# Kernel tuning notes

Hardware: AMD Instinct MI355X
Metric: run time of the kernel (lower is better)

The kernel has to match this reference:

```python
import jax, jax.numpy as jnp
import numpy as np

N = 131072      # total nodes per (sub)graph batch
G = 1024        # number of graphs (= len(data.y))
NPG = N // G    # nodes per graph
E = 4194304     # edges per subgraph (avg degree 32)
D = 128         # input feature dim
LAT = (32, 32, 32)
HID = 128


def setup_inputs() -> dict:
    key = jax.random.key(0)
    ks = jax.random.split(key, 16)
    f = jnp.float32
    inp = {}
    for j in range(3):
        inp[f"x{j}"] = jax.random.normal(ks[j], (N, D), f)
        inp[f"edge_index{j}"] = jax.random.randint(ks[3 + j], (2, E), 0, N)
        inp[f"batch{j}"] = jnp.repeat(jnp.arange(G), NPG)  # sorted graph ids
    inp["y"] = jax.random.randint(ks[6], (G,), 0, 2)
    dims = [D] + list(LAT)
    for i in range(3):
        inp[f"Wc{i}"] = jax.random.normal(ks[7 + i], (dims[i], dims[i + 1]), f) / jnp.sqrt(jnp.asarray(dims[i], f))
        inp[f"bc{i}"] = jnp.zeros((dims[i + 1],), f)
    lat3 = sum(LAT) * 3
    inp["W1"] = jax.random.normal(ks[10], (lat3, HID), f) / jnp.sqrt(jnp.asarray(lat3, f))
    inp["b1"] = jnp.zeros((HID,), f)
    inp["W2"] = jax.random.normal(ks[11], (HID, 2), f) / jnp.sqrt(jnp.asarray(HID, f))
    inp["b2"] = jnp.zeros((2,), f)
    return inp


def gcn_conv(x, edge_index, W, b):
    """torch_geometric GCNConv: add self-loops + symmetric normalization."""
    n = x.shape[0]
    h = x @ W                                   # [N, out]
    src, dst = edge_index[0], edge_index[1]
    ones = jnp.ones(src.shape[0], h.dtype)
    deg = jax.ops.segment_sum(ones, dst, num_segments=n) + 1.0  # +1 self-loop
    dis = jax.lax.rsqrt(deg)                    # deg^{-1/2}
    norm = dis[src] * dis[dst]                  # [E]
    agg = jax.ops.segment_sum(h[src] * norm[:, None], dst, num_segments=n)
    return agg + h * (dis * dis)[:, None] + b   # self-loop term = h/deg


def branch(x, edge_index, batch, convs):
    h = x
    outs = []
    for (W, b) in convs:
        h = jnp.tanh(gcn_conv(h, edge_index, W, b))
        outs.append(h)
    feat = jnp.concatenate(outs, axis=1)        # [N, 96]
    # first node index of each graph (batch is sorted)
    idx = jnp.searchsorted(batch, jnp.arange(batch.shape[0] // NPG * 0 + G))
    return feat[idx]                            # [G, 96]


def reference(x0, edge_index0, batch0, x1, edge_index1, batch1,
              x2, edge_index2, batch2, y,
              Wc0, bc0, Wc1, bc1, Wc2, bc2, W1, b1, W2, b2):
    convs = [(Wc0, bc0), (Wc1, bc1), (Wc2, bc2)]  # shared across subgraphs
    feats = [branch(x, ei, b, convs)
             for (x, ei, b) in ((x0, edge_index0, batch0),
                                (x1, edge_index1, batch1),
                                (x2, edge_index2, batch2))]
    cat = jnp.concatenate(feats, axis=1)        # [G, 288]
    hidden = cat @ W1 + b1                      # [G, HID]
    feature = hidden
    h = jax.nn.relu(hidden)
    logits = jax.nn.log_softmax(h @ W2 + b2, axis=1)  # [G, 2]
    loss = -jnp.mean(logits[jnp.arange(G), y])  # nll_loss
    pred = jnp.argmax(logits, axis=1)
    acc = jnp.mean((pred == y).astype(jnp.float32))
    return logits, loss, acc, feature
```

## Files before the change

### kernel.cpp

```cpp
#include <hip/hip_runtime.h>
#include <hip/hip_bf16.h>
#include <hip/hip_fp16.h>

#define NN  131072
#define GG  1024
#define NPG 128
#define EE  4194304
#define DD  128
#define CC  32
#define NB  512
#define BTILE 4096
#define CAP 9600

typedef __hip_bfloat16 bf16;

__global__ void k_probe(const unsigned short* __restrict__ x, int* __restrict__ flag) {
    unsigned short u = x[threadIdx.x];
    int e = (u >> 7) & 0xFF;
    int q = (e >= 0x70 && e <= 0x85) ? 1 : 0;
    unsigned long long m = __ballot(q);
    __shared__ int cnt[2];
    if ((threadIdx.x & 63) == 0) cnt[threadIdx.x >> 6] = __popcll(m);
    __syncthreads();
    if (threadIdx.x == 0) flag[0] = (cnt[0] + cnt[1] >= 96) ? 1 : 0;
}

struct PtrPack { const void* p[10]; };
__global__ void k_cvtall(PtrPack pk, float* __restrict__ wf, const int* __restrict__ flag) {
    int i = blockIdx.x * 256 + threadIdx.x;
    if (i >= 43490) return;
    const int off[11] = {0, 4096, 4128, 5152, 5184, 6208, 6240, 43104, 43232, 43488, 43490};
    int seg = 0;
    #pragma unroll
    for (int k = 1; k < 11; k++) if (i >= off[k]) seg = k;
    int local = i - off[seg];
    if (flag[0]) wf[i] = __bfloat162float(((const bf16*)pk.p[seg])[local]);
    else         wf[i] = ((const float*)pk.p[seg])[local];
}


__global__ void __launch_bounds__(256) k_hist(const int* __restrict__ ei, int* __restrict__ bhist) {
    __shared__ int h[NB];
    int tid = threadIdx.x;
    h[tid] = 0; h[tid + 256] = 0;
    __syncthreads();
    long t0 = (long)blockIdx.x * 8192;
    #pragma unroll 4
    for (int k = 0; k < 32; k++) {
        int e = t0 + k * 256 + tid;
        atomicAdd(&h[ei[EE + e] >> 8], 1);
    }
    __syncthreads();
    atomicAdd(&bhist[tid], h[tid]);
    atomicAdd(&bhist[tid + 256], h[tid + 256]);
}

__global__ void __launch_bounds__(512) k_bscan(const int* __restrict__ bhist,
                                               int* __restrict__ bbase, int* __restrict__ bcur) {
    __shared__ int s[NB];
    int tid = threadIdx.x;
    int v = bhist[tid];
    s[tid] = v;
    __syncthreads();
    for (int o = 1; o < NB; o <<= 1) {
        int t = (tid >= o) ? s[tid - o] : 0;
        __syncthreads();
        s[tid] += t;
        __syncthreads();
    }
    bbase[tid] = s[tid] - v;
    bcur[tid] = s[tid] - v;
    if (tid == NB - 1) bbase[NB] = s[NB - 1];
}

__global__ void __launch_bounds__(512) k_bin(const int* __restrict__ ei,
                                             int* __restrict__ bcur, int2* __restrict__ ebuf) {
    __shared__ int hist[NB], loff[NB], gbase[NB], cur[NB];
    __shared__ int2 staged[BTILE];
    int tid = threadIdx.x;
    long t0 = (long)blockIdx.x * BTILE;
    hist[tid] = 0;
    __syncthreads();
    int sreg[BTILE / 512], dreg[BTILE / 512];
    #pragma unroll
    for (int k = 0; k < BTILE / 512; k++) {
        int e = t0 + k * 512 + tid;
        sreg[k] = ei[e];
        dreg[k] = ei[EE + e];
        atomicAdd(&hist[dreg[k] >> 8], 1);
    }
    __syncthreads();
    int v = hist[tid];
    loff[tid] = v;
    __syncthreads();
    for (int o = 1; o < NB; o <<= 1) {
        int t = (tid >= o) ? loff[tid - o] : 0;
        __syncthreads();
        loff[tid] += t;
        __syncthreads();
    }
    gbase[tid] = atomicAdd(&bcur[tid], v);
    cur[tid] = 0;
    int excl = loff[tid] - v;
    __syncthreads();
    loff[tid] = excl;
    __syncthreads();
    #pragma unroll
    for (int k = 0; k < BTILE / 512; k++) {
        int b = dreg[k] >> 8;
        int r = atomicAdd(&cur[b], 1);
        staged[loff[b] + r] = make_int2(dreg[k], sreg[k]);
    }
    __syncthreads();
    #pragma unroll
    for (int k = 0; k < BTILE / 512; k++) {
        int t = k * 512 + tid;
        int2 p = staged[t];
        int b = p.x >> 8;
        ebuf[gbase[b] + (t - loff[b])] = p;
    }
}

__global__ void __launch_bounds__(256) k_csr(const int* __restrict__ bbase,
                                             const int2* __restrict__ ebuf,
                                             int* __restrict__ rowptr, int* __restrict__ col,
                                             float* __restrict__ dis, int* __restrict__ mark) {
    __shared__ int hist[256], off[256], cur[256];
    __shared__ int lout[CAP];
    int b = blockIdx.x, tid = threadIdx.x;
    int base = bbase[b];
    int n = bbase[b + 1] - base;
    hist[tid] = 0;
    __syncthreads();
    for (int t = tid; t < n; t += 256) {
        int2 p = ebuf[base + t];
        atomicAdd(&hist[p.x & 255], 1);
    }
    __syncthreads();
    int deg = hist[tid];
    off[tid] = deg;
    __syncthreads();
    for (int o = 1; o < 256; o <<= 1) {
        int t = (tid >= o) ? off[tid - o] : 0;
        __syncthreads();
        off[tid] += t;
        __syncthreads();
    }
    int excl = off[tid] - deg;
    int node = b * 256 + tid;
    rowptr[node] = base + excl;
    dis[node] = rsqrtf((float)deg + 1.0f);
    if (b == 0 && tid == 0) rowptr[NN] = EE;
    cur[tid] = 0;
    __syncthreads();
    off[tid] = excl;
    __syncthreads();
    bool fits = (n <= CAP);
    for (int t = tid; t < n; t += 256) {
        int2 p = ebuf[base + t];
        int d8 = p.x & 255;
        int r = off[d8] + atomicAdd(&cur[d8], 1);
        if (fits) lout[r] = p.y;
        else      col[base + r] = p.y;
        if ((p.x & (NPG - 1)) == 0) mark[p.y] = 1;
    }
    __syncthreads();
    if (fits) for (int t = tid; t < n; t += 256) col[base + t] = lout[t];
}

__global__ void k_compact(const int* __restrict__ mark, int* __restrict__ flist,
                          int* __restrict__ fcnt) {
    int i = blockIdx.x * 256 + threadIdx.x;
    if (((i & (NPG - 1)) == 0) || mark[i]) flist[atomicAdd(fcnt, 1)] = i;
}


__device__ __forceinline__ void store_h4(__half* __restrict__ h, long idx, float4 v, float d) {
    union { __half2 h2[2]; uint2 u; } pk;
    pk.h2[0] = __floats2half2_rn(v.x * d, v.y * d);
    pk.h2[1] = __floats2half2_rn(v.z * d, v.w * d);
    *reinterpret_cast<uint2*>(h + idx) = pk.u;
}

#define XPAD0 132

__global__ void __launch_bounds__(256) k_gemm0(const void* __restrict__ x,
                                               const float* __restrict__ W,
                                               __half* __restrict__ h,
                                               const float* __restrict__ dis,
                                               const int* __restrict__ flag) {
    __shared__ float Wl[DD * CC];
    __shared__ float xl[32 * XPAD0];
    int tid = threadIdx.x;
    long rowbase = (long)blockIdx.x * 32;
    const float4* W4 = (const float4*)W;
    float4* Wl4 = (float4*)Wl;
    for (int t = tid; t < DD * CC / 4; t += 256) Wl4[t] = W4[t];
    if (flag[0]) {
        const uint2* xv = (const uint2*)((const unsigned short*)x + rowbase * DD);
        for (int t = tid; t < 1024; t += 256) {
            uint2 u = xv[t];
            float4 v;
            v.x = __uint_as_float(u.x << 16);
            v.y = __uint_as_float(u.x & 0xffff0000u);
            v.z = __uint_as_float(u.y << 16);
            v.w = __uint_as_float(u.y & 0xffff0000u);
            *(float4*)&xl[(t >> 5) * XPAD0 + (t & 31) * 4] = v;
        }
    } else {
        const float4* xv = (const float4*)((const float*)x + rowbase * DD);
        for (int t = tid; t < 1024; t += 256)
            *(float4*)&xl[(t >> 5) * XPAD0 + (t & 31) * 4] = xv[t];
    }
    __syncthreads();
    int r = tid >> 3, c4 = tid & 7;
    float4 acc = make_float4(0.f, 0.f, 0.f, 0.f);
    const float* xr = &xl[r * XPAD0];
    #pragma unroll 8
    for (int k = 0; k < DD; k++) {
        float xv = xr[k];
        float4 wv = Wl4[k * 8 + c4];
        acc.x += xv * wv.x; acc.y += xv * wv.y;
        acc.z += xv * wv.z; acc.w += xv * wv.w;
    }
    long row = rowbase + r;
    store_h4(h, row * CC + c4 * 4, acc, dis[row]);
}

#define XPAD1 36

__global__ void __launch_bounds__(256) k_gemm32(const float* __restrict__ hin,
                                                const float* __restrict__ W,
                                                __half* __restrict__ hout,
                                                const float* __restrict__ dis) {
    __shared__ float Wl[CC * CC];
    __shared__ float xl[32 * XPAD1];
    int tid = threadIdx.x;
    long rowbase = (long)blockIdx.x * 32;
    float4* Wl4 = (float4*)Wl;
    if (tid < 256) Wl4[tid] = ((const float4*)W)[tid];
    {
        int r = tid >> 3, j = tid & 7;
        float4 v = ((const float4*)hin)[(rowbase + r) * 8 + j];
        *(float4*)&xl[r * XPAD1 + j * 4] = v;
    }
    __syncthreads();
    int r = tid >> 3, c4 = tid & 7;
    float4 acc = make_float4(0.f, 0.f, 0.f, 0.f);
    const float* xr = &xl[r * XPAD1];
    #pragma unroll
    for (int k = 0; k < CC; k++) {
        float xv = xr[k];
        float4 wv = Wl4[k * 8 + c4];
        acc.x += xv * wv.x; acc.y += xv * wv.y;
        acc.z += xv * wv.z; acc.w += xv * wv.w;
    }
    long row = rowbase + r;
    store_h4(hout, row * CC + c4 * 4, acc, dis[row]);
}

__global__ void __launch_bounds__(256) k_gemm32l(const float* __restrict__ hin,
                                                 const float* __restrict__ W,
                                                 __half* __restrict__ hout,
                                                 const float* __restrict__ dis,
                                                 const int* __restrict__ flist,
                                                 const int* __restrict__ fcnt) {
    int n = *fcnt;
    int base = blockIdx.x * 32;
    if (base >= n) return;
    __shared__ float Wl[CC * CC];
    __shared__ float xl[32 * XPAD1];
    __shared__ int rows[32];
    int tid = threadIdx.x;
    float4* Wl4 = (float4*)Wl;
    if (tid < 256) Wl4[tid] = ((const float4*)W)[tid];
    if (tid < 32) rows[tid] = (base + tid < n) ? flist[base + tid] : flist[n - 1];
    __syncthreads();
    {
        int r = tid >> 3, j = tid & 7;
        float4 v = ((const float4*)hin)[(long)rows[r] * 8 + j];
        *(float4*)&xl[r * XPAD1 + j * 4] = v;
    }
    __syncthreads();
    int r = tid >> 3, c4 = tid & 7;
    float4 acc = make_float4(0.f, 0.f, 0.f, 0.f);
    const float* xr = &xl[r * XPAD1];
    #pragma unroll
    for (int k = 0; k < CC; k++) {
        float xv = xr[k];
        float4 wv = Wl4[k * 8 + c4];
        acc.x += xv * wv.x; acc.y += xv * wv.y;
        acc.z += xv * wv.z; acc.w += xv * wv.w;
    }
    long row = rows[r];
    store_h4(hout, row * CC + c4 * 4, acc, dis[row]);
}


__device__ __forceinline__ void acc_h4(float2 raw, float& ax, float& ay,
                                       float& az, float& aw) {
    __half2* h = reinterpret_cast<__half2*>(&raw);
    float2 a = __half22float2(h[0]);
    float2 b = __half22float2(h[1]);
    ax += a.x; ay += a.y; az += b.x; aw += b.y;
}

__device__ __forceinline__ float4 gat_row4(const int* __restrict__ col,
                                           const float2* __restrict__ pb,
                                           int r0, int r1, int p, int q) {
    float ax = 0.f, ay = 0.f, az = 0.f, aw = 0.f;
    int e = r0 + p;
    for (; e + 8 < r1; e += 16) {
        int s0 = col[e], s1 = col[e + 8];
        float2 v0 = pb[(long)s0 * 8 + q];
        float2 v1 = pb[(long)s1 * 8 + q];
        acc_h4(v0, ax, ay, az, aw);
        acc_h4(v1, ax, ay, az, aw);
    }
    if (e < r1) {
        float2 v = pb[(long)col[e] * 8 + q];
        acc_h4(v, ax, ay, az, aw);
    }
    #pragma unroll
    for (int m = 8; m < 64; m <<= 1) {
        ax += __shfl_xor(ax, m);
        ay += __shfl_xor(ay, m);
        az += __shfl_xor(az, m);
        aw += __shfl_xor(aw, m);
    }
    return make_float4(ax, ay, az, aw);
}

__device__ __forceinline__ void gat_write(const float* __restrict__ dis,
                                          const float2* __restrict__ pb,
                                          const float* __restrict__ bias,
                                          float* __restrict__ hbuf,
                                          float* __restrict__ cat, int boff,
                                          int d, int q, float4 acc, bool wr_h) {
    float dd = dis[d];
    float sx = 0.f, sy = 0.f, sz = 0.f, sw = 0.f;
    acc_h4(pb[(long)d * 8 + q], sx, sy, sz, sw);
    float4 bq = ((const float4*)bias)[q];
    float4 v;
    v.x = tanhf((acc.x + sx) * dd + bq.x);
    v.y = tanhf((acc.y + sy) * dd + bq.y);
    v.z = tanhf((acc.z + sz) * dd + bq.z);
    v.w = tanhf((acc.w + sw) * dd + bq.w);
    if (wr_h) ((float4*)hbuf)[(long)d * 8 + q] = v;
    if ((d & (NPG - 1)) == 0) ((float4*)(cat + (d >> 7) * 288 + boff))[q] = v;
}

__global__ void __launch_bounds__(256) k_gat_all(const int* __restrict__ rowptr,
                                                 const int* __restrict__ col,
                                                 const float* __restrict__ dis,
                                                 const __half* __restrict__ pbuf,
                                                 const float* __restrict__ bias,
                                                 float* __restrict__ hbuf,
                                                 float* __restrict__ cat, int boff) {
    int tid = threadIdx.x;
    int d = blockIdx.x * 4 + (tid >> 6);
    int p = (tid >> 3) & 7, q = tid & 7;
    int r0 = rowptr[d], r1 = rowptr[d + 1];
    const float2* pb = (const float2*)pbuf;
    float4 acc = gat_row4(col, pb, r0, r1, p, q);
    if (p == 0) gat_write(dis, pb, bias, hbuf, cat, boff, d, q, acc, true);
}

__global__ void __launch_bounds__(256) k_gat_list(const int* __restrict__ rowptr,
                                                  const int* __restrict__ col,
                                                  const float* __restrict__ dis,
                                                  const __half* __restrict__ pbuf,
                                                  const float* __restrict__ bias,
                                                  float* __restrict__ hbuf,
                                                  float* __restrict__ cat, int boff,
                                                  const int* __restrict__ flist,
                                                  const int* __restrict__ fcnt) {
    int tid = threadIdx.x;
    int idx = blockIdx.x * 4 + (tid >> 6);
    if (idx >= *fcnt) return;
    int d = flist[idx];
    int p = (tid >> 3) & 7, q = tid & 7;
    int r0 = rowptr[d], r1 = rowptr[d + 1];
    const float2* pb = (const float2*)pbuf;
    float4 acc = gat_row4(col, pb, r0, r1, p, q);
    if (p == 0) gat_write(dis, pb, bias, hbuf, cat, boff, d, q, acc, true);
}

__global__ void __launch_bounds__(256) k_gat_seed(const int* __restrict__ rowptr,
                                                  const int* __restrict__ col,
                                                  const float* __restrict__ dis,
                                                  const __half* __restrict__ pbuf,
                                                  const float* __restrict__ bias,
                                                  float* __restrict__ cat, int boff) {
    int tid = threadIdx.x;
    int g = blockIdx.x * 4 + (tid >> 6);
    int d = g * NPG;
    int p = (tid >> 3) & 7, q = tid & 7;
    int r0 = rowptr[d], r1 = rowptr[d + 1];
    const float2* pb = (const float2*)pbuf;
    float4 acc = gat_row4(col, pb, r0, r1, p, q);
    if (p == 0) gat_write(dis, pb, bias, nullptr, cat, boff, d, q, acc, false);
}

__global__ void __launch_bounds__(128) k_head(const float* __restrict__ cat,
                                              const float* __restrict__ W1,
                                              const float* __restrict__ b1,
                                              const float* __restrict__ W2,
                                              const float* __restrict__ b2,
                                              const int* __restrict__ y,
                                              void* __restrict__ out,
                                              float* __restrict__ scal,
                                              const int* __restrict__ flag) {
    __shared__ float crow[288];
    __shared__ float red[4];
    int g = blockIdx.x, tid = threadIdx.x;
    int bfm = flag[0];
    for (int t = tid; t < 288; t += 128) crow[t] = cat[g * 288 + t];
    __syncthreads();
    float acc = 0.f;
    #pragma unroll 4
    for (int k = 0; k < 288; k++) acc += crow[k] * W1[k * 128 + tid];
    acc += b1[tid];
    if (bfm) ((bf16*)out)[2050 + g * 128 + tid] = __float2bfloat16(acc);
    else     ((float*)out)[2050 + g * 128 + tid] = acc;
    float r = fmaxf(acc, 0.f);
    float p0 = r * W2[tid * 2 + 0];
    float p1 = r * W2[tid * 2 + 1];
    for (int o = 32; o > 0; o >>= 1) {
        p0 += __shfl_down(p0, o);
        p1 += __shfl_down(p1, o);
    }
    if ((tid & 63) == 0) { red[(tid >> 6) * 2 + 0] = p0; red[(tid >> 6) * 2 + 1] = p1; }
    __syncthreads();
    if (tid == 0) {
        float l0 = red[0] + red[2] + b2[0];
        float l1 = red[1] + red[3] + b2[1];
        float m = fmaxf(l0, l1);
        float lse = m + logf(expf(l0 - m) + expf(l1 - m));
        float g0 = l0 - lse, g1 = l1 - lse;
        if (bfm) {
            ((bf16*)out)[g * 2 + 0] = __float2bfloat16(g0);
            ((bf16*)out)[g * 2 + 1] = __float2bfloat16(g1);
        } else {
            ((float*)out)[g * 2 + 0] = g0;
            ((float*)out)[g * 2 + 1] = g1;
        }
        int yy = y[g];
        atomicAdd(&scal[0], (yy == 0) ? -g0 : -g1);
        int pred = (l1 > l0) ? 1 : 0;
        if (pred == yy) atomicAdd(&scal[1], 1.0f);
    }
}

__global__ void k_fin(const float* __restrict__ scal, void* __restrict__ out,
                      const int* __restrict__ flag) {
    if (threadIdx.x == 0 && blockIdx.x == 0) {
        if (flag[0]) {
            ((bf16*)out)[2048] = __float2bfloat16(scal[0] / (float)GG);
            ((bf16*)out)[2049] = __float2bfloat16(scal[1] / (float)GG);
        } else {
            ((float*)out)[2048] = scal[0] / (float)GG;
            ((float*)out)[2049] = scal[1] / (float)GG;
        }
    }
}

extern "C" void kernel_launch(void* const* d_in, const int* in_sizes, int n_in,
                              void* d_out, int out_size, void* d_ws, size_t ws_size,
                              hipStream_t stream) {
    const void* x[3]  = {d_in[0], d_in[3], d_in[6]};
    const int*  ei[3] = {(const int*)d_in[1], (const int*)d_in[4], (const int*)d_in[7]};
    const int*  y     = (const int*)d_in[9];

    int*   rowptr = (int*)d_ws;
    int*   col    = rowptr + NN + 2;
    int*   mark   = col + EE;
    int*   flist  = mark + NN;
    int*   fcnt   = flist + NN;
    int*   bhist  = fcnt + 1;
    int*   bbase  = bhist + 512;
    int*   bcur   = bbase + 513;
    float* dis    = (float*)(bcur + 512);
    float* pbuf   = dis + NN;
    float* hbuf   = pbuf + (size_t)NN * CC;
    int2*  ebuf   = (int2*)pbuf;
    __half* pbufh = (__half*)pbuf;
    float* cat    = hbuf + (size_t)NN * CC;
    float* scal   = cat + (size_t)GG * 288;
    int*   flag   = (int*)(scal + 2);
    float* wf     = (float*)(flag + 2);
    float* fWc0 = wf;
    float* fbc0 = wf + 4096;
    float* fWc1 = wf + 4128;
    float* fbc1 = wf + 5152;
    float* fWc2 = wf + 5184;
    float* fbc2 = wf + 6208;
    float* fW1  = wf + 6240;
    float* fb1  = wf + 43104;
    float* fW2  = wf + 43232;
    float* fb2  = wf + 43488;
    size_t need = (size_t)((char*)(wf + 43490) - (char*)d_ws);
    if (ws_size < need) return;

    k_probe<<<1, 128, 0, stream>>>((const unsigned short*)x[0], flag);
    PtrPack pk;
    for (int k = 0; k < 10; k++) pk.p[k] = d_in[10 + k];
    k_cvtall<<<170, 256, 0, stream>>>(pk, wf, flag);
    hipMemsetAsync(scal, 0, 2 * sizeof(float), stream);

    const float* fW[3] = {fWc0, fWc1, fWc2};
    const float* fb[3] = {fbc0, fbc1, fbc2};

    for (int b = 0; b < 3; b++) {
        hipMemsetAsync(bhist, 0, NB * sizeof(int), stream);
        hipMemsetAsync(mark, 0, NN * sizeof(int), stream);
        hipMemsetAsync(fcnt, 0, sizeof(int), stream);
        k_hist<<<512, 256, 0, stream>>>(ei[b], bhist);
        k_bscan<<<1, 512, 0, stream>>>(bhist, bbase, bcur);
        k_bin<<<EE / BTILE, 512, 0, stream>>>(ei[b], bcur, ebuf);
        k_csr<<<NB, 256, 0, stream>>>(bbase, ebuf, rowptr, col, dis, mark);
        k_compact<<<NN / 256, 256, 0, stream>>>(mark, flist, fcnt);

        k_gemm0<<<NN / 32, 256, 0, stream>>>(x[b], fW[0], pbufh, dis, flag);
        k_gat_all<<<NN / 4, 256, 0, stream>>>(rowptr, col, dis, pbufh, fb[0], hbuf, cat, b * 96);
        k_gemm32<<<NN / 32, 256, 0, stream>>>(hbuf, fW[1], pbufh, dis);
        k_gat_list<<<NN / 4, 256, 0, stream>>>(rowptr, col, dis, pbufh, fb[1], hbuf, cat,
                                               b * 96 + 32, flist, fcnt);
        k_gemm32l<<<NN / 32, 256, 0, stream>>>(hbuf, fW[2], pbufh, dis, flist, fcnt);
        k_gat_seed<<<GG / 4, 256, 0, stream>>>(rowptr, col, dis, pbufh, fb[2], cat, b * 96 + 64);
    }

    k_head<<<GG, 128, 0, stream>>>(cat, fW1, fb1, fW2, fb2, y, d_out, scal, flag);
    k_fin<<<1, 64, 0, stream>>>(scal, d_out, flag);
}
```

Measured before the change: 1.182 ms.

## Fuse next-layer 32x32 GEMM into gather kernels and use nontemporal loads

The per-row tanh output of each aggregation kernel is now multiplied by the next layer's weight matrix inside the same kernel using wavefront shuffles, and written directly as a half-precision pre-scaled buffer. This removes the separate k_gemm32/k_gemm32l launches and the fp32 hbuf round trip. Ping-pong buffers avoid read/write hazards. Nontemporal loads are added for x and the CSR column indices to reduce cache pollution. The cost is extra shuffle work and a weight load into shared memory in every gather block.

```diff
diff --git a/kernel.cpp b/kernel.cpp
--- a/kernel.cpp
+++ b/kernel.cpp
@@ -197,20 +197,31 @@
     float4* Wl4 = (float4*)Wl;
     for (int t = tid; t < DD * CC / 4; t += 256) Wl4[t] = W4[t];
     if (flag[0]) {
-        const uint2* xv = (const uint2*)((const unsigned short*)x + rowbase * DD);
+        const unsigned long long* xv =
+            (const unsigned long long*)((const unsigned short*)x + rowbase * DD);
         for (int t = tid; t < 1024; t += 256) {
-            uint2 u = xv[t];
+            unsigned long long u = __builtin_nontemporal_load(xv + t);
+            unsigned int lo = (unsigned int)u, hi = (unsigned int)(u >> 32);
             float4 v;
-            v.x = __uint_as_float(u.x << 16);
-            v.y = __uint_as_float(u.x & 0xffff0000u);
-            v.z = __uint_as_float(u.y << 16);
-            v.w = __uint_as_float(u.y & 0xffff0000u);
+            v.x = __uint_as_float(lo << 16);
+            v.y = __uint_as_float(lo & 0xffff0000u);
+            v.z = __uint_as_float(hi << 16);
+            v.w = __uint_as_float(hi & 0xffff0000u);
             *(float4*)&xl[(t >> 5) * XPAD0 + (t & 31) * 4] = v;
         }
     } else {
-        const float4* xv = (const float4*)((const float*)x + rowbase * DD);
-        for (int t = tid; t < 1024; t += 256)
-            *(float4*)&xl[(t >> 5) * XPAD0 + (t & 31) * 4] = xv[t];
+        const unsigned long long* xv =
+            (const unsigned long long*)((const float*)x + rowbase * DD);
+        for (int t = tid; t < 1024; t += 256) {
+            unsigned long long a = __builtin_nontemporal_load(xv + 2 * t);
+            unsigned long long b = __builtin_nontemporal_load(xv + 2 * t + 1);
+            float4 v;
+            v.x = __uint_as_float((unsigned int)a);
+            v.y = __uint_as_float((unsigned int)(a >> 32));
+            v.z = __uint_as_float((unsigned int)b);
+            v.w = __uint_as_float((unsigned int)(b >> 32));
+            *(float4*)&xl[(t >> 5) * XPAD0 + (t & 31) * 4] = v;
+        }
     }
     __syncthreads();
     int r = tid >> 3, c4 = tid & 7;
@@ -227,75 +238,6 @@
     store_h4(h, row * CC + c4 * 4, acc, dis[row]);
 }
 
-#define XPAD1 36
-
-__global__ void __launch_bounds__(256) k_gemm32(const float* __restrict__ hin,
-                                                const float* __restrict__ W,
-                                                __half* __restrict__ hout,
-                                                const float* __restrict__ dis) {
-    __shared__ float Wl[CC * CC];
-    __shared__ float xl[32 * XPAD1];
-    int tid = threadIdx.x;
-    long rowbase = (long)blockIdx.x * 32;
-    float4* Wl4 = (float4*)Wl;
-    if (tid < 256) Wl4[tid] = ((const float4*)W)[tid];
-    {
-        int r = tid >> 3, j = tid & 7;
-        float4 v = ((const float4*)hin)[(rowbase + r) * 8 + j];
-        *(float4*)&xl[r * XPAD1 + j * 4] = v;
-    }
-    __syncthreads();
-    int r = tid >> 3, c4 = tid & 7;
-    float4 acc = make_float4(0.f, 0.f, 0.f, 0.f);
-    const float* xr = &xl[r * XPAD1];
-    #pragma unroll
-    for (int k = 0; k < CC; k++) {
-        float xv = xr[k];
-        float4 wv = Wl4[k * 8 + c4];
-        acc.x += xv * wv.x; acc.y += xv * wv.y;
-        acc.z += xv * wv.z; acc.w += xv * wv.w;
-    }
-    long row = rowbase + r;
-    store_h4(hout, row * CC + c4 * 4, acc, dis[row]);
-}
-
-__global__ void __launch_bounds__(256) k_gemm32l(const float* __restrict__ hin,
-                                                 const float* __restrict__ W,
-                                                 __half* __restrict__ hout,
-                                                 const float* __restrict__ dis,
-                                                 const int* __restrict__ flist,
-                                                 const int* __restrict__ fcnt) {
-    int n = *fcnt;
-    int base = blockIdx.x * 32;
-    if (base >= n) return;
-    __shared__ float Wl[CC * CC];
-    __shared__ float xl[32 * XPAD1];
-    __shared__ int rows[32];
-    int tid = threadIdx.x;
-    float4* Wl4 = (float4*)Wl;
-    if (tid < 256) Wl4[tid] = ((const float4*)W)[tid];
-    if (tid < 32) rows[tid] = (base + tid < n) ? flist[base + tid] : flist[n - 1];
-    __syncthreads();
-    {
-        int r = tid >> 3, j = tid & 7;
-        float4 v = ((const float4*)hin)[(long)rows[r] * 8 + j];
-        *(float4*)&xl[r * XPAD1 + j * 4] = v;
-    }
-    __syncthreads();
-    int r = tid >> 3, c4 = tid & 7;
-    float4 acc = make_float4(0.f, 0.f, 0.f, 0.f);
-    const float* xr = &xl[r * XPAD1];
-    #pragma unroll
-    for (int k = 0; k < CC; k++) {
-        float xv = xr[k];
-        float4 wv = Wl4[k * 8 + c4];
-        acc.x += xv * wv.x; acc.y += xv * wv.y;
-        acc.z += xv * wv.z; acc.w += xv * wv.w;
-    }
-    long row = rows[r];
-    store_h4(hout, row * CC + c4 * 4, acc, dis[row]);
-}
-
 
 __device__ __forceinline__ void acc_h4(float2 raw, float& ax, float& ay,
                                        float& az, float& aw) {
@@ -311,14 +253,16 @@
     float ax = 0.f, ay = 0.f, az = 0.f, aw = 0.f;
     int e = r0 + p;
     for (; e + 8 < r1; e += 16) {
-        int s0 = col[e], s1 = col[e + 8];
+        int s0 = __builtin_nontemporal_load(col + e);
+        int s1 = __builtin_nontemporal_load(col + e + 8);
         float2 v0 = pb[(long)s0 * 8 + q];
         float2 v1 = pb[(long)s1 * 8 + q];
         acc_h4(v0, ax, ay, az, aw);
         acc_h4(v1, ax, ay, az, aw);
     }
     if (e < r1) {
-        float2 v = pb[(long)col[e] * 8 + q];
+        int s = __builtin_nontemporal_load(col + e);
+        float2 v = pb[(long)s * 8 + q];
         acc_h4(v, ax, ay, az, aw);
     }
     #pragma unroll
@@ -331,13 +275,14 @@
     return make_float4(ax, ay, az, aw);
 }
 
-__device__ __forceinline__ void gat_write(const float* __restrict__ dis,
-                                          const float2* __restrict__ pb,
-                                          const float* __restrict__ bias,
-                                          float* __restrict__ hbuf,
-                                          float* __restrict__ cat, int boff,
-                                          int d, int q, float4 acc, bool wr_h) {
-    float dd = dis[d];
+__device__ __forceinline__ float4 gat_v(const int* __restrict__ col,
+                                        const float2* __restrict__ pb,
+                                        const float* __restrict__ dis,
+                                        const float* __restrict__ bias,
+                                        int d, int r0, int r1, int p, int q,
+                                        float& dd) {
+    float4 acc = gat_row4(col, pb, r0, r1, p, q);
+    dd = dis[d];
     float sx = 0.f, sy = 0.f, sz = 0.f, sw = 0.f;
     acc_h4(pb[(long)d * 8 + q], sx, sy, sz, sw);
     float4 bq = ((const float4*)bias)[q];
@@ -346,8 +291,29 @@
     v.y = tanhf((acc.y + sy) * dd + bq.y);
     v.z = tanhf((acc.z + sz) * dd + bq.z);
     v.w = tanhf((acc.w + sw) * dd + bq.w);
-    if (wr_h) ((float4*)hbuf)[(long)d * 8 + q] = v;
-    if ((d & (NPG - 1)) == 0) ((float4*)(cat + (d >> 7) * 288 + boff))[q] = v;
+    return v;
+}
+
+__device__ __forceinline__ void gat_next(const float* __restrict__ Wl,
+                                         float4 v, float dd,
+                                         __half* __restrict__ pn, int d, int lane) {
+    int cc = lane & 31, hf = lane >> 5;
+    float o = 0.f;
+    #pragma unroll
+    for (int i = 0; i < 16; i++) {
+        int src = 4 * hf + (i >> 2);
+        float xv;
+        if ((i & 3) == 0)      xv = __shfl(v.x, src);
+        else if ((i & 3) == 1) xv = __shfl(v.y, src);
+        else if ((i & 3) == 2) xv = __shfl(v.z, src);
+        else                   xv = __shfl(v.w, src);
+        o += xv * Wl[(16 * hf + i) * 33 + cc];
+    }
+    o += __shfl_xor(o, 32);
+    float pv = o * dd;
+    float rv = __shfl_xor(pv, 1);
+    if (lane < 32 && !(lane & 1))
+        *(__half2*)(pn + (long)d * 32 + cc) = __floats2half2_rn(pv, rv);
 }
 
 __global__ void __launch_bounds__(256) k_gat_all(const int* __restrict__ rowptr,
@@ -355,15 +321,23 @@
                                                  const float* __restrict__ dis,
                                                  const __half* __restrict__ pbuf,
                                                  const float* __restrict__ bias,
-                                                 float* __restrict__ hbuf,
+                                                 const float* __restrict__ Wn,
+                                                 __half* __restrict__ pn,
                                                  float* __restrict__ cat, int boff) {
-    int tid = threadIdx.x;
+    __shared__ float Wl[32 * 33];
+    int tid = threadIdx.x;
+    for (int t = tid; t < 1024; t += 256) Wl[(t >> 5) * 33 + (t & 31)] = Wn[t];
+    __syncthreads();
     int d = blockIdx.x * 4 + (tid >> 6);
-    int p = (tid >> 3) & 7, q = tid & 7;
+    int lane = tid & 63;
+    int p = lane >> 3, q = lane & 7;
     int r0 = rowptr[d], r1 = rowptr[d + 1];
     const float2* pb = (const float2*)pbuf;
-    float4 acc = gat_row4(col, pb, r0, r1, p, q);
-    if (p == 0) gat_write(dis, pb, bias, hbuf, cat, boff, d, q, acc, true);
+    float dd;
+    float4 v = gat_v(col, pb, dis, bias, d, r0, r1, p, q, dd);
+    if (p == 0 && (d & (NPG - 1)) == 0)
+        ((float4*)(cat + (d >> 7) * 288 + boff))[q] = v;
+    gat_next(Wl, v, dd, pn, d, lane);
 }
 
 __global__ void __launch_bounds__(256) k_gat_list(const int* __restrict__ rowptr,
@@ -371,19 +345,29 @@
                                                   const float* __restrict__ dis,
                                                   const __half* __restrict__ pbuf,
                                                   const float* __restrict__ bias,
-                                                  float* __restrict__ hbuf,
+                                                  const float* __restrict__ Wn,
+                                                  __half* __restrict__ pn,
                                                   float* __restrict__ cat, int boff,
                                                   const int* __restrict__ flist,
                                                   const int* __restrict__ fcnt) {
-    int tid = threadIdx.x;
+    __shared__ float Wl[32 * 33];
+    int tid = threadIdx.x;
+    int nf = *fcnt;
+    if (blockIdx.x * 4 >= nf) return;
+    for (int t = tid; t < 1024; t += 256) Wl[(t >> 5) * 33 + (t & 31)] = Wn[t];
+    __syncthreads();
     int idx = blockIdx.x * 4 + (tid >> 6);
-    if (idx >= *fcnt) return;
+    if (idx >= nf) return;
     int d = flist[idx];
-    int p = (tid >> 3) & 7, q = tid & 7;
+    int lane = tid & 63;
+    int p = lane >> 3, q = lane & 7;
     int r0 = rowptr[d], r1 = rowptr[d + 1];
     const float2* pb = (const float2*)pbuf;
-    float4 acc = gat_row4(col, pb, r0, r1, p, q);
-    if (p == 0) gat_write(dis, pb, bias, hbuf, cat, boff, d, q, acc, true);
+    float dd;
+    float4 v = gat_v(col, pb, dis, bias, d, r0, r1, p, q, dd);
+    if (p == 0 && (d & (NPG - 1)) == 0)
+        ((float4*)(cat + (d >> 7) * 288 + boff))[q] = v;
+    gat_next(Wl, v, dd, pn, d, lane);
 }
 
 __global__ void __launch_bounds__(256) k_gat_seed(const int* __restrict__ rowptr,
@@ -395,11 +379,13 @@
     int tid = threadIdx.x;
     int g = blockIdx.x * 4 + (tid >> 6);
     int d = g * NPG;
-    int p = (tid >> 3) & 7, q = tid & 7;
+    int lane = tid & 63;
+    int p = lane >> 3, q = lane & 7;
     int r0 = rowptr[d], r1 = rowptr[d + 1];
     const float2* pb = (const float2*)pbuf;
-    float4 acc = gat_row4(col, pb, r0, r1, p, q);
-    if (p == 0) gat_write(dis, pb, bias, nullptr, cat, boff, d, q, acc, false);
+    float dd;
+    float4 v = gat_v(col, pb, dis, bias, d, r0, r1, p, q, dd);
+    if (p == 0) ((float4*)(cat + g * 288 + boff))[q] = v;
 }
 
 __global__ void __launch_bounds__(128) k_head(const float* __restrict__ cat,
@@ -484,7 +470,8 @@
     float* pbuf   = dis + NN;
     float* hbuf   = pbuf + (size_t)NN * CC;
     int2*  ebuf   = (int2*)pbuf;
-    __half* pbufh = (__half*)pbuf;
+    __half* pbufA = (__half*)pbuf;
+    __half* pbufB = pbufA + (size_t)NN * CC;
     float* cat    = hbuf + (size_t)NN * CC;
     float* scal   = cat + (size_t)GG * 288;
     int*   flag   = (int*)(scal + 2);
@@ -508,9 +495,6 @@
     k_cvtall<<<170, 256, 0, stream>>>(pk, wf, flag);
     hipMemsetAsync(scal, 0, 2 * sizeof(float), stream);
 
-    const float* fW[3] = {fWc0, fWc1, fWc2};
-    const float* fb[3] = {fbc0, fbc1, fbc2};
-
     for (int b = 0; b < 3; b++) {
         hipMemsetAsync(bhist, 0, NB * sizeof(int), stream);
         hipMemsetAsync(mark, 0, NN * sizeof(int), stream);
@@ -521,13 +505,14 @@
         k_csr<<<NB, 256, 0, stream>>>(bbase, ebuf, rowptr, col, dis, mark);
         k_compact<<<NN / 256, 256, 0, stream>>>(mark, flist, fcnt);
 
-        k_gemm0<<<NN / 32, 256, 0, stream>>>(x[b], fW[0], pbufh, dis, flag);
-        k_gat_all<<<NN / 4, 256, 0, stream>>>(rowptr, col, dis, pbufh, fb[0], hbuf, cat, b * 96);
-        k_gemm32<<<NN / 32, 256, 0, stream>>>(hbuf, fW[1], pbufh, dis);
-        k_gat_list<<<NN / 4, 256, 0, stream>>>(rowptr, col, dis, pbufh, fb[1], hbuf, cat,
-                                               b * 96 + 32, flist, fcnt);
-        k_gemm32l<<<NN / 32, 256, 0, stream>>>(hbuf, fW[2], pbufh, dis, flist, fcnt);
-        k_gat_seed<<<GG / 4, 256, 0, stream>>>(rowptr, col, dis, pbufh, fb[2], cat, b * 96 + 64);
+        k_gemm0<<<NN / 32, 256, 0, stream>>>(x[b], fWc0, pbufA, dis, flag);
+        k_gat_all<<<NN / 4, 256, 0, stream>>>(rowptr, col, dis, pbufA, fbc0,
+                                              fWc1, pbufB, cat, b * 96);
+        k_gat_list<<<NN / 4, 256, 0, stream>>>(rowptr, col, dis, pbufB, fbc1,
+                                               fWc2, pbufA, cat, b * 96 + 32,
+                                               flist, fcnt);
+        k_gat_seed<<<GG / 4, 256, 0, stream>>>(rowptr, col, dis, pbufA, fbc2,
+                                               cat, b * 96 + 64);
     }
 
     k_head<<<GG, 128, 0, stream>>>(cat, fW1, fb1, fW2, fb2, y, d_out, scal, flag);
```

Result: slower. 1.224 ms (+3.5%).
